# Kernel tuning notes

Hardware: AMD Instinct MI355X
Metric: run time of the kernel (lower is better)

The kernel has to match this reference:

```python
import jax, jax.numpy as jnp
import numpy as np

H, C = 4, 64            # heads, hidden_channels (per-head dim, concat=False)
N_SRC = N_TGT = 50000
E = 400000
E_LBL = 200000
NEG_SLOPE = 0.2
LN_EPS = 1e-5


def _gatv2(x_src, x_dst, ei, Wl, bl, Wr, br, att, bias, n_dst):
    # PyG GATv2Conv, bipartite, add_self_loops=False, concat=False (mean over heads)
    xl = (x_src @ Wl.T + bl).reshape(x_src.shape[0], H, C)   # lin_l(x_src)
    xr = (x_dst @ Wr.T + br).reshape(x_dst.shape[0], H, C)   # lin_r(x_dst)
    s, d = ei[0], ei[1]
    e = jax.nn.leaky_relu(xl[s] + xr[d], NEG_SLOPE)          # [E,H,C]
    logits = jnp.einsum('ehc,hc->eh', e, att)                # [E,H]
    m = jax.ops.segment_max(logits, d, num_segments=n_dst)
    m = jnp.where(jnp.isfinite(m), m, 0.0)                   # empty segments -> 0
    ex = jnp.exp(logits - m[d])
    den = jax.ops.segment_sum(ex, d, num_segments=n_dst)
    alpha = ex / (den[d] + 1e-16)                            # segment softmax over dst
    out = jax.ops.segment_sum(xl[s] * alpha[:, :, None], d, num_segments=n_dst)
    return out.mean(axis=1) + bias                           # [n_dst, C]


def _layer_norm(x, w, b):
    mu = x.mean(-1, keepdims=True)
    v = ((x - mu) ** 2).mean(-1, keepdims=True)
    return (x - mu) / jnp.sqrt(v + LN_EPS) * w + b


def setup_inputs() -> dict:
    key = jax.random.key(0)
    ks = iter(jax.random.split(key, 64))
    def p(shape, scale=0.1):
        return jax.random.normal(next(ks), shape, jnp.float32) * scale
    inp = {}
    inp['src_emb'] = p((N_SRC, C))
    inp['tgt_emb'] = p((N_TGT, C))
    for name in ['c1st', 'c1ts', 'c2st', 'c2ts']:
        inp[name + '_Wl'] = p((H * C, C))
        inp[name + '_bl'] = jnp.zeros((H * C,), jnp.float32)
        inp[name + '_Wr'] = p((H * C, C))
        inp[name + '_br'] = jnp.zeros((H * C,), jnp.float32)
        inp[name + '_att'] = p((H, C))
        inp[name + '_bias'] = jnp.zeros((C,), jnp.float32)
    inp['ln_s_w'] = jnp.ones((C,), jnp.float32)
    inp['ln_s_b'] = jnp.zeros((C,), jnp.float32)
    inp['ln_t_w'] = jnp.ones((C,), jnp.float32)
    inp['ln_t_b'] = jnp.zeros((C,), jnp.float32)
    inp['node_id_source'] = jnp.arange(N_SRC)
    inp['node_id_target'] = jnp.arange(N_TGT)
    inp['edge_index_st'] = jax.random.randint(next(ks), (2, E), 0, N_SRC)
    inp['edge_index_ts'] = jax.random.randint(next(ks), (2, E), 0, N_TGT)
    inp['edge_label_index'] = jax.random.randint(next(ks), (2, E_LBL), 0, N_SRC)
    return inp


def reference(src_emb, tgt_emb,
              c1st_Wl, c1st_bl, c1st_Wr, c1st_br, c1st_att, c1st_bias,
              c1ts_Wl, c1ts_bl, c1ts_Wr, c1ts_br, c1ts_att, c1ts_bias,
              c2st_Wl, c2st_bl, c2st_Wr, c2st_br, c2st_att, c2st_bias,
              c2ts_Wl, c2ts_bl, c2ts_Wr, c2ts_br, c2ts_att, c2ts_bias,
              ln_s_w, ln_s_b, ln_t_w, ln_t_b,
              node_id_source, node_id_target,
              edge_index_st, edge_index_ts, edge_label_index):
    x_s = src_emb[node_id_source]
    x_t = tgt_emb[node_id_target]
    # layer 1 (to_hetero: one conv per edge type, sum-aggregate per node type)
    h_t = _gatv2(x_s, x_t, edge_index_st, c1st_Wl, c1st_bl, c1st_Wr, c1st_br, c1st_att, c1st_bias, N_TGT)
    h_s = _gatv2(x_t, x_s, edge_index_ts, c1ts_Wl, c1ts_bl, c1ts_Wr, c1ts_br, c1ts_att, c1ts_bias, N_SRC)
    h_s = _layer_norm(jax.nn.relu(h_s), ln_s_w, ln_s_b)
    h_t = _layer_norm(jax.nn.relu(h_t), ln_t_w, ln_t_b)
    # layer 2
    o_t = _gatv2(h_s, h_t, edge_index_st, c2st_Wl, c2st_bl, c2st_Wr, c2st_br, c2st_att, c2st_bias, N_TGT)
    o_s = _gatv2(h_t, h_s, edge_index_ts, c2ts_Wl, c2ts_bl, c2ts_Wr, c2ts_br, c2ts_att, c2ts_bias, N_SRC)
    # classifier: edge-wise dot product
    pred = (o_s[edge_label_index[0]] * o_t[edge_label_index[1]]).sum(axis=-1)
    return pred
```

## Files before the change

kernel.cpp:

```cpp
#include <hip/hip_runtime.h>

#define NEG_SLOPE 0.2f
#define LN_EPS 1e-5f

typedef __attribute__((ext_vector_type(8))) short bf16x8;
typedef __attribute__((ext_vector_type(4))) float f32x4;

__device__ __forceinline__ short f2bf(float f) {
    unsigned u = __float_as_uint(f);
    return (short)((u + 0x7FFFu + ((u >> 16) & 1u)) >> 16);
}
__device__ __forceinline__ float bf2f(unsigned short s) {
    return __uint_as_float(((unsigned)s) << 16);
}

#define DPP_ADD(v, ctrl) \
    v += __int_as_float(__builtin_amdgcn_update_dpp(0, __float_as_int(v), ctrl, 0xF, 0xF, true))
__device__ __forceinline__ float dpp_sum16(float v) {
    DPP_ADD(v, 0xB1);
    DPP_ADD(v, 0x4E);
    DPP_ADD(v, 0x141);
    DPP_ADD(v, 0x140);
    return v;
}

struct LinJob {
    const float* x; const int* ids; const float* W; const float* bias;
    unsigned short* out; int n;
};
struct LinJob4 { LinJob j[4]; };

__global__ __launch_bounds__(256) void lin4_kernel(LinJob4 P, int bpj)
{
    int jid = blockIdx.x / bpj;
    LinJob job = P.j[jid];
    int blk = blockIdx.x - jid * bpj;
    const float* __restrict__ x = job.x;
    const int* __restrict__ ids = job.ids;
    const float* __restrict__ W = job.W;
    int n = job.n;

    int wv = threadIdx.x >> 6;
    int lane = threadIdx.x & 63;
    int m = lane & 15, q = lane >> 4;
    bf16x8 wfrag[4][2];
#pragma unroll
    for (int t = 0; t < 4; ++t) {
        int ncol = wv * 64 + t * 16 + m;
        const float* wr = W + ncol * 64 + q * 8;
#pragma unroll
        for (int h = 0; h < 2; ++h) {
            const float4* p = (const float4*)(wr + h * 32);
            float4 u = p[0], v = p[1];
            bf16x8 f;
            f[0]=f2bf(u.x); f[1]=f2bf(u.y); f[2]=f2bf(u.z); f[3]=f2bf(u.w);
            f[4]=f2bf(v.x); f[5]=f2bf(v.y); f[6]=f2bf(v.z); f[7]=f2bf(v.w);
            wfrag[t][h] = f;
        }
    }
    float4 biasv[4];
#pragma unroll
    for (int t = 0; t < 4; ++t)
        biasv[t] = *(const float4*)(job.bias + wv * 64 + t * 16 + q * 4);

    int ntiles = (n + 15) >> 4;
    for (int tile = blk; tile < ntiles; tile += bpj) {
        int row = tile * 16 + m;
        int rc = row < n ? row : n - 1;
        int src = ids ? ids[rc] : rc;
        const float* xr = x + (size_t)src * 64 + q * 8;
        bf16x8 xfrag[2];
#pragma unroll
        for (int h = 0; h < 2; ++h) {
            const float4* p = (const float4*)(xr + h * 32);
            float4 u = p[0], v = p[1];
            bf16x8 f;
            f[0]=f2bf(u.x); f[1]=f2bf(u.y); f[2]=f2bf(u.z); f[3]=f2bf(u.w);
            f[4]=f2bf(v.x); f[5]=f2bf(v.y); f[6]=f2bf(v.z); f[7]=f2bf(v.w);
            xfrag[h] = f;
        }
        bool valid = row < n;
        unsigned short* orow = job.out + (size_t)row * 256 + wv * 64 + q * 4;
#pragma unroll
        for (int t = 0; t < 4; ++t) {
            f32x4 acc = {0.f, 0.f, 0.f, 0.f};
            acc = __builtin_amdgcn_mfma_f32_16x16x32_bf16(wfrag[t][0], xfrag[0], acc, 0, 0, 0);
            acc = __builtin_amdgcn_mfma_f32_16x16x32_bf16(wfrag[t][1], xfrag[1], acc, 0, 0, 0);
            if (valid) {
                ushort4 o;
                o.x = (unsigned short)f2bf(acc[0] + biasv[t].x);
                o.y = (unsigned short)f2bf(acc[1] + biasv[t].y);
                o.z = (unsigned short)f2bf(acc[2] + biasv[t].z);
                o.w = (unsigned short)f2bf(acc[3] + biasv[t].w);
                *(ushort4*)(orow + t * 16) = o;
            }
        }
    }
}

__global__ __launch_bounds__(256) void hist2_kernel(
    const int* __restrict__ ed0, int E0, int* __restrict__ cnt0,
    const int* __restrict__ ed1, int E1, int* __restrict__ cnt1)
{
    int i = blockIdx.x * 256 + threadIdx.x;
    if (i < E0) atomicAdd(&cnt0[ed0[i]], 1);
    else { int k = i - E0; if (k < E1) atomicAdd(&cnt1[ed1[k]], 1); }
}

__global__ __launch_bounds__(256) void chunk_sum2_kernel(
    const int* __restrict__ cnt0, int* __restrict__ csum0, int n0, int nc0,
    const int* __restrict__ cnt1, int* __restrict__ csum1, int n1)
{
    const int* cnt; int* csum; int n; int blk;
    if (blockIdx.x < (unsigned)nc0) { cnt = cnt0; csum = csum0; n = n0; blk = blockIdx.x; }
    else { cnt = cnt1; csum = csum1; n = n1; blk = blockIdx.x - nc0; }
    __shared__ int wsm[4];
    int tid = threadIdx.x;
    int base = blk * 1024 + tid * 4;
    int s = 0;
#pragma unroll
    for (int k = 0; k < 4; ++k) { int i = base + k; if (i < n) s += cnt[i]; }
#pragma unroll
    for (int ofs = 32; ofs > 0; ofs >>= 1) s += __shfl_xor(s, ofs, 64);
    if ((tid & 63) == 0) wsm[tid >> 6] = s;
    __syncthreads();
    if (tid == 0) csum[blk] = wsm[0] + wsm[1] + wsm[2] + wsm[3];
}

__global__ __launch_bounds__(128) void chunk_scan2_kernel(
    int* __restrict__ c0, int n0, int* __restrict__ c1, int n1)
{
    int w = threadIdx.x >> 6, lane = threadIdx.x & 63;
    int* c = w ? c1 : c0;
    int n = w ? n1 : n0;
    int v = (lane < n) ? c[lane] : 0;
    int incl = v;
#pragma unroll
    for (int ofs = 1; ofs < 64; ofs <<= 1) {
        int t = __shfl_up(incl, ofs, 64);
        if (lane >= ofs) incl += t;
    }
    if (lane < n) c[lane] = incl - v;
}

__global__ __launch_bounds__(1024) void scan_apply2_kernel(
    const int* __restrict__ cnt0, const int* __restrict__ co0, int* __restrict__ offs0, int n0, int nc0,
    const int* __restrict__ cnt1, const int* __restrict__ co1, int* __restrict__ offs1, int n1)
{
    const int* cnt; const int* co; int* offs; int n; int blk;
    if (blockIdx.x < (unsigned)nc0) { cnt = cnt0; co = co0; offs = offs0; n = n0; blk = blockIdx.x; }
    else { cnt = cnt1; co = co1; offs = offs1; n = n1; blk = blockIdx.x - nc0; }
    __shared__ int wsum[16];
    int tid = threadIdx.x, lane = tid & 63, w = tid >> 6;
    int i = blk * 1024 + tid;
    int v = (i < n) ? cnt[i] : 0;
    int incl = v;
#pragma unroll
    for (int ofs = 1; ofs < 64; ofs <<= 1) {
        int t = __shfl_up(incl, ofs, 64);
        if (lane >= ofs) incl += t;
    }
    if (lane == 63) wsum[w] = incl;
    __syncthreads();
    if (w == 0) {
        int x = (lane < 16) ? wsum[lane] : 0;
#pragma unroll
        for (int ofs = 1; ofs < 16; ofs <<= 1) {
            int t = __shfl_up(x, ofs, 64);
            if (lane >= ofs) x += t;
        }
        if (lane < 16) wsum[lane] = x;
    }
    __syncthreads();
    int woff = (w == 0) ? 0 : wsum[w - 1];
    if (i < n) offs[i + 1] = co[blk] + woff + incl;
    if (i == 0) offs[0] = 0;
}

__global__ __launch_bounds__(256) void fill2_kernel(
    const int* __restrict__ es0, const int* __restrict__ ed0,
    const int* __restrict__ offs0, int* __restrict__ cur0, int* __restrict__ srt0, int E0,
    const int* __restrict__ es1, const int* __restrict__ ed1,
    const int* __restrict__ offs1, int* __restrict__ cur1, int* __restrict__ srt1, int E1)
{
    int i = blockIdx.x * 256 + threadIdx.x;
    if (i < E0) {
        int d = ed0[i];
        int pos = offs0[d] + atomicAdd(&cur0[d], 1);
        srt0[pos] = es0[i];
    } else {
        int k = i - E0;
        if (k < E1) {
            int d = ed1[k];
            int pos = offs1[d] + atomicAdd(&cur1[d], 1);
            srt1[pos] = es1[k];
        }
    }
}

struct GatJob {
    const unsigned short* A; const unsigned short* B;
    const int* offs; const int* srt;
    const float* att; const float* bias;
    const float* lnw; const float* lnb;
    float* out; int n_dst;
};

__global__ __launch_bounds__(256) void gat2_kernel(GatJob j0, GatJob j1, int blocks0)
{
    GatJob job = (blockIdx.x < (unsigned)blocks0) ? j0 : j1;
    int blk = (blockIdx.x < (unsigned)blocks0) ? blockIdx.x : blockIdx.x - blocks0;
    int d = blk * 4 + (threadIdx.x >> 6);
    int lane = threadIdx.x & 63;
    if (d >= job.n_dst) return;
    int g = lane & 15;
    const unsigned short* __restrict__ A = job.A;
    float4 att4 = ((const float4*)job.att)[lane];
    ushort4 bu = ((const ushort4*)(job.B + (size_t)d * 256))[lane];
    float4 br4 = {bf2f(bu.x), bf2f(bu.y), bf2f(bu.z), bf2f(bu.w)};

    float den1 = 0.f, den2 = 0.f;
    float4 acc1 = {0,0,0,0}, acc2 = {0,0,0,0};
    const int* __restrict__ srt = job.srt;
    int j0i = job.offs[d], j1i = job.offs[d + 1];
    int j = j0i;

#define EDGE_LOAD(S, AR) \
    ushort4 u##AR = ((const ushort4*)(A + (size_t)(S) * 256))[lane]; \
    float4 AR = {bf2f(u##AR.x), bf2f(u##AR.y), bf2f(u##AR.z), bf2f(u##AR.w)};
#define EDGE_LOGIT(AR, P) \
    float P; { \
        float tx = AR.x + br4.x; tx = tx > 0.f ? tx : NEG_SLOPE * tx; \
        float ty = AR.y + br4.y; ty = ty > 0.f ? ty : NEG_SLOPE * ty; \
        float tz = AR.z + br4.z; tz = tz > 0.f ? tz : NEG_SLOPE * tz; \
        float tw = AR.w + br4.w; tw = tw > 0.f ? tw : NEG_SLOPE * tw; \
        P = tx * att4.x + ty * att4.y + tz * att4.z + tw * att4.w; }
#define EDGE_ACC(AR, P, DEN, ACC) { \
        float pe = __expf(P); \
        DEN += pe; \
        ACC.x = fmaf(pe, AR.x, ACC.x); \
        ACC.y = fmaf(pe, AR.y, ACC.y); \
        ACC.z = fmaf(pe, AR.z, ACC.z); \
        ACC.w = fmaf(pe, AR.w, ACC.w); }

    for (; j + 1 < j1i; j += 2) {
        int s0 = srt[j], s1 = srt[j + 1];
        EDGE_LOAD(s0, a0) EDGE_LOAD(s1, a1)
        EDGE_LOGIT(a0, p0) EDGE_LOGIT(a1, p1)
        p0 = dpp_sum16(p0);
        p1 = dpp_sum16(p1);
        EDGE_ACC(a0, p0, den1, acc1) EDGE_ACC(a1, p1, den2, acc2)
    }
    if (j < j1i) {
        int s0 = srt[j];
        EDGE_LOAD(s0, a0)
        EDGE_LOGIT(a0, p0)
        p0 = dpp_sum16(p0);
        EDGE_ACC(a0, p0, den1, acc1)
    }
#undef EDGE_LOAD
#undef EDGE_LOGIT
#undef EDGE_ACC

    float den = den1 + den2;
    float4 acc;
    acc.x = acc1.x + acc2.x;
    acc.y = acc1.y + acc2.y;
    acc.z = acc1.z + acc2.z;
    acc.w = acc1.w + acc2.w;
    float inv = 1.f / (den + 1e-16f);
    acc.x *= inv; acc.y *= inv; acc.z *= inv; acc.w *= inv;
    acc.x += __shfl_xor(acc.x, 16, 64);
    acc.y += __shfl_xor(acc.y, 16, 64);
    acc.z += __shfl_xor(acc.z, 16, 64);
    acc.w += __shfl_xor(acc.w, 16, 64);
    acc.x += __shfl_xor(acc.x, 32, 64);
    acc.y += __shfl_xor(acc.y, 32, 64);
    acc.z += __shfl_xor(acc.z, 32, 64);
    acc.w += __shfl_xor(acc.w, 32, 64);
    float4 b4 = ((const float4*)job.bias)[g];
    float4 v;
    v.x = acc.x * 0.25f + b4.x;
    v.y = acc.y * 0.25f + b4.y;
    v.z = acc.z * 0.25f + b4.z;
    v.w = acc.w * 0.25f + b4.w;
    if (job.lnw) {
        v.x = v.x > 0.f ? v.x : 0.f;
        v.y = v.y > 0.f ? v.y : 0.f;
        v.z = v.z > 0.f ? v.z : 0.f;
        v.w = v.w > 0.f ? v.w : 0.f;
        float s  = dpp_sum16(v.x + v.y + v.z + v.w);
        float ss = dpp_sum16(v.x*v.x + v.y*v.y + v.z*v.z + v.w*v.w);
        float mu = s * (1.f / 64.f);
        float var = ss * (1.f / 64.f) - mu * mu;
        float rs = rsqrtf(var + LN_EPS);
        float4 w4 = ((const float4*)job.lnw)[g];
        float4 l4 = ((const float4*)job.lnb)[g];
        v.x = (v.x - mu) * rs * w4.x + l4.x;
        v.y = (v.y - mu) * rs * w4.y + l4.y;
        v.z = (v.z - mu) * rs * w4.z + l4.z;
        v.w = (v.w - mu) * rs * w4.w + l4.w;
    }
    if (lane < 16) ((float4*)(job.out + (size_t)d * 64))[g] = v;
}

__global__ __launch_bounds__(256) void dot_kernel(
    const float* __restrict__ os, const float* __restrict__ ot,
    const int* __restrict__ ea, const int* __restrict__ eb,
    float* __restrict__ out, int n)
{
    int e = (int)((blockIdx.x * 256u + threadIdx.x) >> 4);
    int l = threadIdx.x & 15;
    if (e >= n) return;
    float4 a = ((const float4*)(os + (size_t)ea[e] * 64))[l];
    float4 b = ((const float4*)(ot + (size_t)eb[e] * 64))[l];
    float v = dpp_sum16(a.x * b.x + a.y * b.y + a.z * b.z + a.w * b.w);
    if (l == 0) out[e] = v;
}

extern "C" void kernel_launch(void* const* d_in, const int* in_sizes, int n_in,
                              void* d_out, int out_size, void* d_ws, size_t ws_size,
                              hipStream_t stream)
{
    const float* src_emb = (const float*)d_in[0];
    const float* tgt_emb = (const float*)d_in[1];
    const float* P[4][6];
    for (int ci = 0; ci < 4; ++ci)
        for (int k = 0; k < 6; ++k)
            P[ci][k] = (const float*)d_in[2 + ci * 6 + k];
    const float* ln_s_w = (const float*)d_in[26];
    const float* ln_s_b = (const float*)d_in[27];
    const float* ln_t_w = (const float*)d_in[28];
    const float* ln_t_b = (const float*)d_in[29];
    const int* nid_s = (const int*)d_in[30];
    const int* nid_t = (const int*)d_in[31];
    const int* ei_st = (const int*)d_in[32];
    const int* ei_ts = (const int*)d_in[33];
    const int* eli   = (const int*)d_in[34];

    int n_src = in_sizes[30];
    int n_tgt = in_sizes[31];
    int E_st = in_sizes[32] / 2;
    int E_ts = in_sizes[33] / 2;
    int EL   = in_sizes[34] / 2;
    int nmax = n_src > n_tgt ? n_src : n_tgt;

    float* ws = (float*)d_ws;
    size_t off = 0;
    auto alloc = [&](size_t count) {
        float* p = ws + off;
        off += (count + 63) & ~(size_t)63;
        return p;
    };
    unsigned short* A_st = (unsigned short*)alloc((size_t)nmax * 128);
    unsigned short* B_st = (unsigned short*)alloc((size_t)nmax * 128);
    unsigned short* A_ts = (unsigned short*)alloc((size_t)nmax * 128);
    unsigned short* B_ts = (unsigned short*)alloc((size_t)nmax * 128);
    int*   offs_st = (int*)alloc((size_t)n_tgt + 1);
    int*   srt_st  = (int*)alloc((size_t)E_st);
    int*   offs_ts = (int*)alloc((size_t)n_src + 1);
    int*   srt_ts  = (int*)alloc((size_t)E_ts);
    int*   zeros   = (int*)alloc((size_t)4 * nmax);
    int*   csum0   = (int*)alloc(64);
    int*   csum1   = (int*)alloc(64);
    float* h_s     = alloc((size_t)n_src * 64);
    float* h_t     = alloc((size_t)n_tgt * 64);
    float* o_s     = alloc((size_t)n_src * 64);
    float* o_t     = alloc((size_t)n_tgt * 64);
    if (off * sizeof(float) > ws_size) return;

    int* cnt0 = zeros;
    int* cnt1 = zeros + nmax;
    int* cur0 = zeros + 2 * (size_t)nmax;
    int* cur1 = zeros + 3 * (size_t)nmax;

    int nc0 = (n_tgt + 1023) / 1024, nc1 = (n_src + 1023) / 1024;
    hipMemsetAsync(zeros, 0, (size_t)4 * nmax * sizeof(int), stream);
    hist2_kernel<<<(E_st + E_ts + 255) / 256, 256, 0, stream>>>(
        ei_st + E_st, E_st, cnt0, ei_ts + E_ts, E_ts, cnt1);
    chunk_sum2_kernel<<<nc0 + nc1, 256, 0, stream>>>(cnt0, csum0, n_tgt, nc0, cnt1, csum1, n_src);
    chunk_scan2_kernel<<<1, 128, 0, stream>>>(csum0, nc0, csum1, nc1);
    scan_apply2_kernel<<<nc0 + nc1, 1024, 0, stream>>>(
        cnt0, csum0, offs_st, n_tgt, nc0, cnt1, csum1, offs_ts, n_src);
    fill2_kernel<<<(E_st + E_ts + 255) / 256, 256, 0, stream>>>(
        ei_st, ei_st + E_st, offs_st, cur0, srt_st, E_st,
        ei_ts, ei_ts + E_ts, offs_ts, cur1, srt_ts, E_ts);

    int bpj = (nmax + 63) / 64;

    auto lin_layer = [&](const float* xs, const int* ids_s, int ns,
                         const float* xt, const int* ids_t, int nt,
                         const float* const* pst, const float* const* pts) {
        LinJob4 LJ;
        LJ.j[0] = { xs, ids_s, pst[0], pst[1], A_st, ns };
        LJ.j[1] = { xt, ids_t, pst[2], pst[3], B_st, nt };
        LJ.j[2] = { xt, ids_t, pts[0], pts[1], A_ts, nt };
        LJ.j[3] = { xs, ids_s, pts[2], pts[3], B_ts, ns };
        lin4_kernel<<<4 * bpj, 256, 0, stream>>>(LJ, bpj);
    };
    auto gat_layer = [&](const float* const* pst, const float* const* pts,
                         const float* lnw_t, const float* lnb_t,
                         const float* lnw_s, const float* lnb_s,
                         float* out_t, float* out_s) {
        GatJob g0 = { A_st, B_st, offs_st, srt_st, pst[4], pst[5], lnw_t, lnb_t, out_t, n_tgt };
        GatJob g1 = { A_ts, B_ts, offs_ts, srt_ts, pts[4], pts[5], lnw_s, lnb_s, out_s, n_src };
        int b0 = (n_tgt + 3) / 4, b1 = (n_src + 3) / 4;
        gat2_kernel<<<b0 + b1, 256, 0, stream>>>(g0, g1, b0);
    };

    lin_layer(src_emb, nid_s, n_src, tgt_emb, nid_t, n_tgt, P[0], P[1]);
    gat_layer(P[0], P[1], ln_t_w, ln_t_b, ln_s_w, ln_s_b, h_t, h_s);

    lin_layer(h_s, nullptr, n_src, h_t, nullptr, n_tgt, P[2], P[3]);
    gat_layer(P[2], P[3], nullptr, nullptr, nullptr, nullptr, o_t, o_s);

    dot_kernel<<<((size_t)EL * 16 + 255) / 256, 256, 0, stream>>>(
        o_s, o_t, eli, eli + EL, (float*)d_out, EL);
}
```

Measured before the change: 511.1 us.

## Merge CSR scan into one kernel, pack GAT edge math, cap linear grid

```diff
diff --git a/kernel.cpp b/kernel.cpp
--- a/kernel.cpp
+++ b/kernel.cpp
@@ -5,13 +5,11 @@
 
 typedef __attribute__((ext_vector_type(8))) short bf16x8;
 typedef __attribute__((ext_vector_type(4))) float f32x4;
+typedef __attribute__((ext_vector_type(2))) float f32x2;
 
 __device__ __forceinline__ short f2bf(float f) {
     unsigned u = __float_as_uint(f);
     return (short)((u + 0x7FFFu + ((u >> 16) & 1u)) >> 16);
-}
-__device__ __forceinline__ float bf2f(unsigned short s) {
-    return __uint_as_float(((unsigned)s) << 16);
 }
 
 #define DPP_ADD(v, ctrl) \
@@ -22,6 +20,13 @@
     DPP_ADD(v, 0x141);
     DPP_ADD(v, 0x140);
     return v;
+}
+
+__device__ __forceinline__ void unpack4(uint2 w, f32x2& lo, f32x2& hi) {
+    lo.x = __uint_as_float(w.x << 16);
+    lo.y = __uint_as_float(w.x & 0xFFFF0000u);
+    hi.x = __uint_as_float(w.y << 16);
+    hi.y = __uint_as_float(w.y & 0xFFFF0000u);
 }
 
 struct LinJob {
@@ -107,54 +112,20 @@
     else { int k = i - E0; if (k < E1) atomicAdd(&cnt1[ed1[k]], 1); }
 }
 
-__global__ __launch_bounds__(256) void chunk_sum2_kernel(
-    const int* __restrict__ cnt0, int* __restrict__ csum0, int n0, int nc0,
-    const int* __restrict__ cnt1, int* __restrict__ csum1, int n1)
-{
-    const int* cnt; int* csum; int n; int blk;
-    if (blockIdx.x < (unsigned)nc0) { cnt = cnt0; csum = csum0; n = n0; blk = blockIdx.x; }
-    else { cnt = cnt1; csum = csum1; n = n1; blk = blockIdx.x - nc0; }
-    __shared__ int wsm[4];
-    int tid = threadIdx.x;
-    int base = blk * 1024 + tid * 4;
+__global__ __launch_bounds__(1024) void scan2_kernel(
+    const int* __restrict__ cnt0, int* __restrict__ offs0, int n0,
+    const int* __restrict__ cnt1, int* __restrict__ offs1, int n1)
+{
+    const int* __restrict__ cnt = blockIdx.x ? cnt1 : cnt0;
+    int* __restrict__ offs = blockIdx.x ? offs1 : offs0;
+    int n = blockIdx.x ? n1 : n0;
+    int tid = threadIdx.x, lane = tid & 63, w = tid >> 6;
+    int C = (n + 1023) >> 10;
+    int beg = tid * C, end = min(beg + C, n);
     int s = 0;
-#pragma unroll
-    for (int k = 0; k < 4; ++k) { int i = base + k; if (i < n) s += cnt[i]; }
-#pragma unroll
-    for (int ofs = 32; ofs > 0; ofs >>= 1) s += __shfl_xor(s, ofs, 64);
-    if ((tid & 63) == 0) wsm[tid >> 6] = s;
-    __syncthreads();
-    if (tid == 0) csum[blk] = wsm[0] + wsm[1] + wsm[2] + wsm[3];
-}
-
-__global__ __launch_bounds__(128) void chunk_scan2_kernel(
-    int* __restrict__ c0, int n0, int* __restrict__ c1, int n1)
-{
-    int w = threadIdx.x >> 6, lane = threadIdx.x & 63;
-    int* c = w ? c1 : c0;
-    int n = w ? n1 : n0;
-    int v = (lane < n) ? c[lane] : 0;
-    int incl = v;
-#pragma unroll
-    for (int ofs = 1; ofs < 64; ofs <<= 1) {
-        int t = __shfl_up(incl, ofs, 64);
-        if (lane >= ofs) incl += t;
-    }
-    if (lane < n) c[lane] = incl - v;
-}
-
-__global__ __launch_bounds__(1024) void scan_apply2_kernel(
-    const int* __restrict__ cnt0, const int* __restrict__ co0, int* __restrict__ offs0, int n0, int nc0,
-    const int* __restrict__ cnt1, const int* __restrict__ co1, int* __restrict__ offs1, int n1)
-{
-    const int* cnt; const int* co; int* offs; int n; int blk;
-    if (blockIdx.x < (unsigned)nc0) { cnt = cnt0; co = co0; offs = offs0; n = n0; blk = blockIdx.x; }
-    else { cnt = cnt1; co = co1; offs = offs1; n = n1; blk = blockIdx.x - nc0; }
+    for (int i = beg; i < end; ++i) s += cnt[i];
     __shared__ int wsum[16];
-    int tid = threadIdx.x, lane = tid & 63, w = tid >> 6;
-    int i = blk * 1024 + tid;
-    int v = (i < n) ? cnt[i] : 0;
-    int incl = v;
+    int incl = s;
 #pragma unroll
     for (int ofs = 1; ofs < 64; ofs <<= 1) {
         int t = __shfl_up(incl, ofs, 64);
@@ -172,9 +143,10 @@
         if (lane < 16) wsum[lane] = x;
     }
     __syncthreads();
-    int woff = (w == 0) ? 0 : wsum[w - 1];
-    if (i < n) offs[i + 1] = co[blk] + woff + incl;
-    if (i == 0) offs[0] = 0;
+    int pre = incl - s + (w ? wsum[w - 1] : 0);
+    int run = pre;
+    for (int i = beg; i < end; ++i) { run += cnt[i]; offs[i + 1] = run; }
+    if (tid == 0) offs[0] = 0;
 }
 
 __global__ __launch_bounds__(256) void fill2_kernel(
@@ -214,62 +186,51 @@
     int lane = threadIdx.x & 63;
     if (d >= job.n_dst) return;
     int g = lane & 15;
-    const unsigned short* __restrict__ A = job.A;
+    const uint2* __restrict__ A2 = (const uint2*)job.A;
     float4 att4 = ((const float4*)job.att)[lane];
-    ushort4 bu = ((const ushort4*)(job.B + (size_t)d * 256))[lane];
-    float4 br4 = {bf2f(bu.x), bf2f(bu.y), bf2f(bu.z), bf2f(bu.w)};
+    f32x2 att01 = {att4.x, att4.y}, att23 = {att4.z, att4.w};
+    uint2 bw = ((const uint2*)(job.B + (size_t)d * 256))[lane];
+    f32x2 b01, b23; unpack4(bw, b01, b23);
+    const f32x2 z2 = {0.f, 0.f};
 
     float den1 = 0.f, den2 = 0.f;
-    float4 acc1 = {0,0,0,0}, acc2 = {0,0,0,0};
+    f32x2 p01 = z2, p23 = z2, q01 = z2, q23 = z2;
     const int* __restrict__ srt = job.srt;
     int j0i = job.offs[d], j1i = job.offs[d + 1];
     int j = j0i;
 
-#define EDGE_LOAD(S, AR) \
-    ushort4 u##AR = ((const ushort4*)(A + (size_t)(S) * 256))[lane]; \
-    float4 AR = {bf2f(u##AR.x), bf2f(u##AR.y), bf2f(u##AR.z), bf2f(u##AR.w)};
-#define EDGE_LOGIT(AR, P) \
-    float P; { \
-        float tx = AR.x + br4.x; tx = tx > 0.f ? tx : NEG_SLOPE * tx; \
-        float ty = AR.y + br4.y; ty = ty > 0.f ? ty : NEG_SLOPE * ty; \
-        float tz = AR.z + br4.z; tz = tz > 0.f ? tz : NEG_SLOPE * tz; \
-        float tw = AR.w + br4.w; tw = tw > 0.f ? tw : NEG_SLOPE * tw; \
-        P = tx * att4.x + ty * att4.y + tz * att4.z + tw * att4.w; }
-#define EDGE_ACC(AR, P, DEN, ACC) { \
-        float pe = __expf(P); \
+#define EDGE(S, DEN, A01, A23) { \
+        uint2 wbits = A2[(unsigned)((S) * 64 + lane)]; \
+        f32x2 a01, a23; unpack4(wbits, a01, a23); \
+        f32x2 t01 = a01 + b01, t23 = a23 + b23; \
+        f32x2 l01 = __builtin_elementwise_min(t01, z2) * NEG_SLOPE \
+                  + __builtin_elementwise_max(t01, z2); \
+        f32x2 l23 = __builtin_elementwise_min(t23, z2) * NEG_SLOPE \
+                  + __builtin_elementwise_max(t23, z2); \
+        f32x2 dp = l01 * att01 + l23 * att23; \
+        float p = dp.x + dp.y; \
+        p = dpp_sum16(p); \
+        float pe = __expf(p); \
         DEN += pe; \
-        ACC.x = fmaf(pe, AR.x, ACC.x); \
-        ACC.y = fmaf(pe, AR.y, ACC.y); \
-        ACC.z = fmaf(pe, AR.z, ACC.z); \
-        ACC.w = fmaf(pe, AR.w, ACC.w); }
+        A01 = a01 * pe + A01; \
+        A23 = a23 * pe + A23; }
 
     for (; j + 1 < j1i; j += 2) {
         int s0 = srt[j], s1 = srt[j + 1];
-        EDGE_LOAD(s0, a0) EDGE_LOAD(s1, a1)
-        EDGE_LOGIT(a0, p0) EDGE_LOGIT(a1, p1)
-        p0 = dpp_sum16(p0);
-        p1 = dpp_sum16(p1);
-        EDGE_ACC(a0, p0, den1, acc1) EDGE_ACC(a1, p1, den2, acc2)
+        EDGE(s0, den1, p01, p23)
+        EDGE(s1, den2, q01, q23)
     }
     if (j < j1i) {
         int s0 = srt[j];
-        EDGE_LOAD(s0, a0)
-        EDGE_LOGIT(a0, p0)
-        p0 = dpp_sum16(p0);
-        EDGE_ACC(a0, p0, den1, acc1)
-    }
-#undef EDGE_LOAD
-#undef EDGE_LOGIT
-#undef EDGE_ACC
+        EDGE(s0, den1, p01, p23)
+    }
+#undef EDGE
 
     float den = den1 + den2;
-    float4 acc;
-    acc.x = acc1.x + acc2.x;
-    acc.y = acc1.y + acc2.y;
-    acc.z = acc1.z + acc2.z;
-    acc.w = acc1.w + acc2.w;
+    f32x2 A01 = p01 + q01, A23 = p23 + q23;
     float inv = 1.f / (den + 1e-16f);
-    acc.x *= inv; acc.y *= inv; acc.z *= inv; acc.w *= inv;
+    A01 *= inv; A23 *= inv;
+    float4 acc = {A01.x, A01.y, A23.x, A23.y};
     acc.x += __shfl_xor(acc.x, 16, 64);
     acc.y += __shfl_xor(acc.y, 16, 64);
     acc.z += __shfl_xor(acc.z, 16, 64);
@@ -361,8 +322,6 @@
     int*   offs_ts = (int*)alloc((size_t)n_src + 1);
     int*   srt_ts  = (int*)alloc((size_t)E_ts);
     int*   zeros   = (int*)alloc((size_t)4 * nmax);
-    int*   csum0   = (int*)alloc(64);
-    int*   csum1   = (int*)alloc(64);
     float* h_s     = alloc((size_t)n_src * 64);
     float* h_t     = alloc((size_t)n_tgt * 64);
     float* o_s     = alloc((size_t)n_src * 64);
@@ -374,19 +333,15 @@
     int* cur0 = zeros + 2 * (size_t)nmax;
     int* cur1 = zeros + 3 * (size_t)nmax;
 
-    int nc0 = (n_tgt + 1023) / 1024, nc1 = (n_src + 1023) / 1024;
     hipMemsetAsync(zeros, 0, (size_t)4 * nmax * sizeof(int), stream);
     hist2_kernel<<<(E_st + E_ts + 255) / 256, 256, 0, stream>>>(
         ei_st + E_st, E_st, cnt0, ei_ts + E_ts, E_ts, cnt1);
-    chunk_sum2_kernel<<<nc0 + nc1, 256, 0, stream>>>(cnt0, csum0, n_tgt, nc0, cnt1, csum1, n_src);
-    chunk_scan2_kernel<<<1, 128, 0, stream>>>(csum0, nc0, csum1, nc1);
-    scan_apply2_kernel<<<nc0 + nc1, 1024, 0, stream>>>(
-        cnt0, csum0, offs_st, n_tgt, nc0, cnt1, csum1, offs_ts, n_src);
+    scan2_kernel<<<2, 1024, 0, stream>>>(cnt0, offs_st, n_tgt, cnt1, offs_ts, n_src);
     fill2_kernel<<<(E_st + E_ts + 255) / 256, 256, 0, stream>>>(
         ei_st, ei_st + E_st, offs_st, cur0, srt_st, E_st,
         ei_ts, ei_ts + E_ts, offs_ts, cur1, srt_ts, E_ts);
 
-    int bpj = (nmax + 63) / 64;
+    int bpj = 512;
 
     auto lin_layer = [&](const float* xs, const int* ids_s, int ns,
                          const float* xt, const int* ids_t, int nt,
```

New measurement: 563.7 us. 10.3% more time.
